# Kernel optimization log

Hardware: AMD Instinct MI355X
Metric: run time of the kernel (lower is better)

## Reference

```python
import jax, jax.numpy as jnp
import numpy as np

B, C, L, O = 32, 256, 336, 96
K, NLAYERS, DFF = 4, 2, 1024
EPS = 1e-5


def setup_inputs() -> dict:
    key = jax.random.key(0)
    ks = jax.random.split(key, 10)
    s1 = 1.0 / np.sqrt(L)
    s2 = 1.0 / np.sqrt(DFF)
    return {
        "x": jax.random.normal(ks[0], (B, C, L), dtype=jnp.float32),
        "rev_w": jnp.ones((C,), dtype=jnp.float32),
        "rev_b": jnp.zeros((C,), dtype=jnp.float32),
        "W1": jax.random.normal(ks[1], (K, NLAYERS, L, DFF), dtype=jnp.float32) * s1,
        "b1": jnp.zeros((K, NLAYERS, DFF), dtype=jnp.float32),
        "W2": jax.random.normal(ks[2], (K, NLAYERS, DFF, L), dtype=jnp.float32) * s2,
        "b2": jnp.zeros((K, NLAYERS, L), dtype=jnp.float32),
        "Wh": jax.random.normal(ks[3], (K, L, O), dtype=jnp.float32) * s1,
        "bh": jnp.zeros((K, O), dtype=jnp.float32),
        "assign": jax.random.randint(ks[4], (C,), 0, K, dtype=jnp.int32),
    }


def reference(x, rev_w, rev_b, W1, b1, W2, b2, Wh, bh, assign):
    # RevIN norm over the time axis, per instance and per channel. x: [B,C,L]
    mean = jnp.mean(x, axis=-1, keepdims=True)
    std = jnp.sqrt(jnp.var(x, axis=-1, keepdims=True) + EPS)
    xn = (x - mean) / std * rev_w[None, :, None] + rev_b[None, :, None]

    n_clusters = Wh.shape[0]
    n_layers = W1.shape[1]
    out = jnp.zeros(x.shape[:2] + (Wh.shape[-1],), dtype=x.dtype)  # [B,C,O]
    for k in range(n_clusters):
        z = xn  # [B,C,L] time-mixing MLP stack shared across channels
        for l in range(n_layers):
            h = jax.nn.relu(jnp.einsum('bcl,ld->bcd', z, W1[k, l]) + b1[k, l])
            z = z + jnp.einsum('bcd,dl->bcl', h, W2[k, l]) + b2[k, l]
        y = jnp.einsum('bcl,lo->bco', z, Wh[k]) + bh[k]  # [B,C,O]
        out = jnp.where((assign == k)[None, :, None], y, out)

    # RevIN denorm, then transpose to [B, out_len, C]
    out = (out - rev_b[None, :, None]) / rev_w[None, :, None] * std + mean
    return jnp.transpose(out, (0, 2, 1))
```

## Files before the change

### kernel.cpp

```cpp
#include <hip/hip_runtime.h>
#include <math.h>


typedef unsigned short u16;
typedef unsigned int u32;
typedef unsigned long long u64;

constexpr int B = 32, C = 256, L = 336, O = 96, K = 4, NL = 2, DFF = 1024;
constexpr int TM = 32;
constexpr int NTILES = (B * C) / TM;
constexpr int LP = 352;
constexpr int KS1 = LP / 32;
constexpr int KS2 = DFF / 32;
constexpr int NT2 = LP / 16;
constexpr int NTH = O / 16;
constexpr int DC = 512;
constexpr int KSC = DC / 32;
constexpr int NTC = DC / 16;
constexpr int ZBS = 360;
constexpr int HSC = DC + 8;

constexpr int W1FRAGS = (DFF / 16) * KS1 * 64;
constexpr int W2FRAGS = NT2 * KS2 * 64;
constexpr int WHFRAGS = NTH * KS1 * 64;
constexpr int NW1 = W1FRAGS * K * NL;
constexpr int NW2 = W2FRAGS * K * NL;
constexpr int NWH = WHFRAGS * K;
constexpr int NFRAG = NW1 + NW2 + NWH;

typedef __bf16 bf16x8 __attribute__((ext_vector_type(8)));
typedef float f32x4 __attribute__((ext_vector_type(4)));

__device__ __forceinline__ u16 f2bf(float f) {
  union { float f; u32 u; } v;
  v.f = f;
  u32 r = v.u + 0x7fffu + ((v.u >> 16) & 1u);
  return (u16)(r >> 16);
}
__device__ __forceinline__ float bf2f(u16 h) {
  union { u32 u; float f; } v;
  v.u = ((u32)h) << 16;
  return v.f;
}

__global__ __launch_bounds__(256) void build_tables(
    const int* __restrict__ assign, int* __restrict__ meta) {
  __shared__ int wcnt[4][K];
  __shared__ int pre[4][K];
  __shared__ int cofs[K + 1];
  const int tid = threadIdx.x;
  const int w = tid >> 6, lane = tid & 63;
  const int a = assign[tid];
  const u64 below = (1ull << lane) - 1ull;
  int myrank = 0;
#pragma unroll
  for (int k = 0; k < K; ++k) {
    const u64 m = __ballot(a == k);
    if (a == k) myrank = (int)__popcll(m & below);
    if (lane == 0) wcnt[w][k] = (int)__popcll(m);
  }
  __syncthreads();
  if (tid == 0) {
    int tot[K];
    for (int k = 0; k < K; ++k) {
      int s = 0;
      for (int ww = 0; ww < 4; ++ww) {
        pre[ww][k] = s;
        s += wcnt[ww][k];
      }
      tot[k] = s;
    }
    cofs[0] = 0;
    for (int k = 0; k < K; ++k) cofs[k + 1] = cofs[k] + tot[k];
    for (int k = 0; k <= K; ++k) meta[512 + k] = cofs[k];
  }
  __syncthreads();
  const int pos = cofs[a] + pre[w][a] + myrank;
  meta[256 + pos] = tid;
  int k = 0;
  while (k < K - 1 && tid >= cofs[k + 1]) ++k;
  meta[tid] = (k << 16) | ((tid - cofs[k]) * TM);
}

__global__ __launch_bounds__(256) void repack(const float* __restrict__ W1,
                                              const float* __restrict__ W2,
                                              const float* __restrict__ Wh,
                                              u16* __restrict__ wbuf) {
  const int gid = blockIdx.x * 256 + threadIdx.x;
  const int lane = gid & 63;
  const int q = lane >> 4, rm = lane & 15;
  float v[8];
  if (gid < NW1) {
    const int kl = gid / W1FRAGS, rem = gid % W1FRAGS;
    const int nt = rem / (KS1 * 64), ks = (rem / 64) % KS1;
    const int d = nt * 16 + rm, lb = ks * 32 + q * 8;
    const float* src = W1 + (size_t)kl * L * DFF;
#pragma unroll
    for (int j = 0; j < 8; ++j) {
      const int l = lb + j;
      v[j] = (l < L) ? src[(size_t)l * DFF + d] : 0.f;
    }
  } else if (gid < NW1 + NW2) {
    const int g = gid - NW1;
    const int kl = g / W2FRAGS, rem = g % W2FRAGS;
    const int nt = rem / (KS2 * 64), ks = (rem / 64) % KS2;
    const int lcol = nt * 16 + rm, db = ks * 32 + q * 8;
    const float* src = W2 + (size_t)kl * DFF * L;
#pragma unroll
    for (int j = 0; j < 8; ++j)
      v[j] = (lcol < L) ? src[(size_t)(db + j) * L + lcol] : 0.f;
  } else {
    const int g = gid - NW1 - NW2;
    const int kk = g / WHFRAGS, rem = g % WHFRAGS;
    const int nt = rem / (KS1 * 64), ks = (rem / 64) % KS1;
    const int o = nt * 16 + rm, lb = ks * 32 + q * 8;
    const float* src = Wh + (size_t)kk * L * O;
#pragma unroll
    for (int j = 0; j < 8; ++j) {
      const int l = lb + j;
      v[j] = (l < L) ? src[(size_t)l * O + o] : 0.f;
    }
  }
  uint4 w;
  w.x = (u32)f2bf(v[0]) | ((u32)f2bf(v[1]) << 16);
  w.y = (u32)f2bf(v[2]) | ((u32)f2bf(v[3]) << 16);
  w.z = (u32)f2bf(v[4]) | ((u32)f2bf(v[5]) << 16);
  w.w = (u32)f2bf(v[6]) | ((u32)f2bf(v[7]) << 16);
  *(uint4*)(wbuf + (size_t)gid * 8) = w;
}

__global__ __launch_bounds__(512, 4) void mlp_mfma(
    const float* __restrict__ x, const float* __restrict__ rev_w,
    const float* __restrict__ rev_b, const float* __restrict__ b1,
    const float* __restrict__ b2, const float* __restrict__ bh,
    const int* __restrict__ meta, const u16* __restrict__ wbuf,
    float* __restrict__ out) {
  __shared__ __align__(16) u16 zb[TM][ZBS];
  __shared__ __align__(16) u16 Hsh[TM][HSC];
  __shared__ float s_mean[TM], s_std[TM], s_rw[TM], s_rb[TM];
  __shared__ int s_b[TM], s_c[TM];

  const int tid = threadIdx.x;
  const int wid = tid >> 6;
  const int lane = tid & 63;
  const int q = lane >> 4, rm = lane & 15;

  const int swz = (blockIdx.x & 7) * 32 + (blockIdx.x >> 3);
  const int info = meta[swz];
  const int kcl = info >> 16;
  const int rstart = info & 0xffff;
  const int cofs = meta[512 + kcl];
  const int cnt = meta[512 + kcl + 1] - cofs;

  for (int i = 0; i < 4; ++i) {
    const int t = wid * 4 + i;
    const int ri = rstart + t;
    const int b = ri / cnt;
    const int c = meta[256 + cofs + (ri % cnt)];
    const float* xrow = x + (size_t)(b * C + c) * L;
    float v[6], s = 0.f, s2 = 0.f;
#pragma unroll
    for (int jj = 0; jj < 6; ++jj) {
      const int j = lane + jj * 64;
      v[jj] = (j < L) ? xrow[j] : 0.f;
      s += v[jj];
      s2 += v[jj] * v[jj];
    }
#pragma unroll
    for (int off = 32; off > 0; off >>= 1) {
      s += __shfl_down(s, off);
      s2 += __shfl_down(s2, off);
    }
    s = __shfl(s, 0);
    s2 = __shfl(s2, 0);
    const float mean = s * (1.f / L);
    const float var = s2 * (1.f / L) - mean * mean;
    const float stdv = sqrtf(var + 1e-5f);
    const float rstd = 1.f / stdv;
    const float rw = rev_w[c], rb_ = rev_b[c];
#pragma unroll
    for (int jj = 0; jj < 6; ++jj) {
      const int j = lane + jj * 64;
      if (j < L) zb[t][j] = f2bf((v[jj] - mean) * rstd * rw + rb_);
    }
    if (lane < LP - L) zb[t][L + lane] = 0;
    if (lane == 0) {
      s_mean[t] = mean;
      s_std[t] = stdv;
      s_rw[t] = rw;
      s_rb[t] = rb_;
      s_b[t] = b;
      s_c[t] = c;
    }
  }
  __syncthreads();

  f32x4 zm[3][2];
#pragma unroll
  for (int t = 0; t < 3; ++t) {
    const int nt2 = wid + 8 * t;
#pragma unroll
    for (int rg = 0; rg < 2; ++rg) {
      if (nt2 < NT2) {
        const uint2 zw = *(const uint2*)&zb[rm + 16 * rg][nt2 * 16 + q * 4];
        zm[t][rg] = f32x4{bf2f((u16)zw.x), bf2f((u16)(zw.x >> 16)),
                          bf2f((u16)zw.y), bf2f((u16)(zw.y >> 16))};
      } else {
        zm[t][rg] = f32x4{0.f, 0.f, 0.f, 0.f};
      }
    }
  }

  const u16* w1b = wbuf;
  const u16* w2b = wbuf + (size_t)NW1 * 8;
  const u16* whb = wbuf + (size_t)(NW1 + NW2) * 8;

  for (int l = 0; l < NL; ++l) {
    const int kl = kcl * NL + l;
    const u16* W1f = w1b + (size_t)kl * W1FRAGS * 8;
    const u16* W2f = w2b + (size_t)kl * W2FRAGS * 8;
    const float* b1p = b1 + kl * DFF;
    const float* b2p = b2 + kl * L;

    for (int cch = 0; cch < 2; ++cch) {
      {
        const u16* base =
            W1f + ((size_t)(cch * NTC + wid * 4) * (KS1 * 512) + lane * 8);
        bf16x8 a_cur[4], a_nxt[4];
#pragma unroll
        for (int t = 0; t < 4; ++t)
          a_cur[t] = *(const bf16x8*)(base + (size_t)t * (KS1 * 512));
        f32x4 acc[4][2];
#pragma unroll
        for (int t = 0; t < 4; ++t)
#pragma unroll
          for (int rg = 0; rg < 2; ++rg) acc[t][rg] = f32x4{0.f, 0.f, 0.f, 0.f};
#pragma unroll 1
        for (int ks = 0; ks < KS1; ++ks) {
          if (ks + 1 < KS1) {
#pragma unroll
            for (int t = 0; t < 4; ++t)
              a_nxt[t] = *(const bf16x8*)(base + (size_t)t * (KS1 * 512) +
                                          (ks + 1) * 512);
          }
          const bf16x8 zf0 = *(const bf16x8*)&zb[rm][ks * 32 + q * 8];
          const bf16x8 zf1 = *(const bf16x8*)&zb[rm + 16][ks * 32 + q * 8];
#pragma unroll
          for (int t = 0; t < 4; ++t) {
            acc[t][0] = __builtin_amdgcn_mfma_f32_16x16x32_bf16(a_cur[t], zf0,
                                                                acc[t][0], 0, 0, 0);
            acc[t][1] = __builtin_amdgcn_mfma_f32_16x16x32_bf16(a_cur[t], zf1,
                                                                acc[t][1], 0, 0, 0);
          }
#pragma unroll
          for (int t = 0; t < 4; ++t) a_cur[t] = a_nxt[t];
        }
#pragma unroll
        for (int t = 0; t < 4; ++t) {
          const int ntl = wid * 4 + t;
          const float4 bq =
              *(const float4*)(b1p + cch * DC + ntl * 16 + q * 4);
#pragma unroll
          for (int rg = 0; rg < 2; ++rg) {
            uint2 hw;
            hw.x = (u32)f2bf(fmaxf(acc[t][rg][0] + bq.x, 0.f)) |
                   ((u32)f2bf(fmaxf(acc[t][rg][1] + bq.y, 0.f)) << 16);
            hw.y = (u32)f2bf(fmaxf(acc[t][rg][2] + bq.z, 0.f)) |
                   ((u32)f2bf(fmaxf(acc[t][rg][3] + bq.w, 0.f)) << 16);
            *(uint2*)&Hsh[rm + 16 * rg][ntl * 16 + q * 4] = hw;
          }
        }
      }
      __syncthreads();

      {
        const u16* b2base = W2f + ((size_t)(cch * KSC) * 512 + lane * 8);
        bf16x8 w_cur[3], w_nxt[3];
#pragma unroll
        for (int t = 0; t < 3; ++t) {
          const int nt2 = wid + 8 * t;
          if (nt2 < NT2)
            w_cur[t] = *(const bf16x8*)(b2base + (size_t)nt2 * (KS2 * 512));
        }
#pragma unroll 1
        for (int ks = 0; ks < KSC; ++ks) {
          if (ks + 1 < KSC) {
#pragma unroll
            for (int t = 0; t < 3; ++t) {
              const int nt2 = wid + 8 * t;
              if (nt2 < NT2)
                w_nxt[t] = *(const bf16x8*)(b2base + (size_t)nt2 * (KS2 * 512) +
                                            (ks + 1) * 512);
            }
          }
          const bf16x8 hf0 = *(const bf16x8*)&Hsh[rm][ks * 32 + q * 8];
          const bf16x8 hf1 = *(const bf16x8*)&Hsh[rm + 16][ks * 32 + q * 8];
#pragma unroll
          for (int t = 0; t < 3; ++t) {
            if (wid + 8 * t < NT2) {
              zm[t][0] = __builtin_amdgcn_mfma_f32_16x16x32_bf16(w_cur[t], hf0,
                                                                 zm[t][0], 0, 0, 0);
              zm[t][1] = __builtin_amdgcn_mfma_f32_16x16x32_bf16(w_cur[t], hf1,
                                                                 zm[t][1], 0, 0, 0);
            }
          }
#pragma unroll
          for (int t = 0; t < 3; ++t) w_cur[t] = w_nxt[t];
        }
      }
      __syncthreads();
    }

#pragma unroll
    for (int t = 0; t < 3; ++t) {
      const int nt2 = wid + 8 * t;
      if (nt2 < NT2) {
        const int lc = nt2 * 16 + q * 4;
        if (lc < L) {
          const float4 bq = *(const float4*)(b2p + lc);
          zm[t][0][0] += bq.x; zm[t][0][1] += bq.y;
          zm[t][0][2] += bq.z; zm[t][0][3] += bq.w;
          zm[t][1][0] += bq.x; zm[t][1][1] += bq.y;
          zm[t][1][2] += bq.z; zm[t][1][3] += bq.w;
        }
#pragma unroll
        for (int rg = 0; rg < 2; ++rg) {
          uint2 zw;
          zw.x = (u32)f2bf(zm[t][rg][0]) | ((u32)f2bf(zm[t][rg][1]) << 16);
          zw.y = (u32)f2bf(zm[t][rg][2]) | ((u32)f2bf(zm[t][rg][3]) << 16);
          *(uint2*)&zb[rm + 16 * rg][lc] = zw;
        }
      }
    }
    __syncthreads();
  }

  if (wid < NTH) {
    const u16* Whf =
        whb + (size_t)kcl * WHFRAGS * 8 + (size_t)wid * (KS1 * 512) + lane * 8;
    f32x4 acc0 = {0.f, 0.f, 0.f, 0.f}, acc1 = {0.f, 0.f, 0.f, 0.f};
    for (int ks = 0; ks < KS1; ++ks) {
      const bf16x8 af = *(const bf16x8*)(Whf + ks * 512);
      const bf16x8 zf0 = *(const bf16x8*)&zb[rm][ks * 32 + q * 8];
      const bf16x8 zf1 = *(const bf16x8*)&zb[rm + 16][ks * 32 + q * 8];
      acc0 = __builtin_amdgcn_mfma_f32_16x16x32_bf16(af, zf0, acc0, 0, 0, 0);
      acc1 = __builtin_amdgcn_mfma_f32_16x16x32_bf16(af, zf1, acc1, 0, 0, 0);
    }
    const float4 bq = *(const float4*)(bh + kcl * O + wid * 16 + q * 4);
    const float bqa[4] = {bq.x, bq.y, bq.z, bq.w};
#pragma unroll
    for (int rg = 0; rg < 2; ++rg) {
      const int row = rm + 16 * rg;
      const float mean = s_mean[row], stdv = s_std[row];
      const float rw = s_rw[row], rb_ = s_rb[row];
      const int ob = s_b[row], oc = s_c[row];
      const f32x4 acc = rg ? acc1 : acc0;
#pragma unroll
      for (int gg = 0; gg < 4; ++gg) {
        const int o = wid * 16 + q * 4 + gg;
        const float y = acc[gg] + bqa[gg];
        out[((size_t)ob * O + o) * C + oc] = (y - rb_) / rw * stdv + mean;
      }
    }
  }
}

extern "C" void kernel_launch(void* const* d_in, const int* in_sizes, int n_in,
                              void* d_out, int out_size, void* d_ws,
                              size_t ws_size, hipStream_t stream) {
  const float* x = (const float*)d_in[0];
  const float* rev_w = (const float*)d_in[1];
  const float* rev_b = (const float*)d_in[2];
  const float* W1 = (const float*)d_in[3];
  const float* b1 = (const float*)d_in[4];
  const float* W2 = (const float*)d_in[5];
  const float* b2 = (const float*)d_in[6];
  const float* Wh = (const float*)d_in[7];
  const float* bh = (const float*)d_in[8];
  const int* assign = (const int*)d_in[9];
  float* out = (float*)d_out;

  int* meta = (int*)d_ws;
  u16* wbuf = (u16*)((char*)d_ws + 4096);

  build_tables<<<1, 256, 0, stream>>>(assign, meta);
  repack<<<NFRAG / 256, 256, 0, stream>>>(W1, W2, Wh, wbuf);
  mlp_mfma<<<NTILES, 512, 0, stream>>>(x, rev_w, rev_b, b1, b2, bh, meta, wbuf,
                                       out);
}
```

Measured before the change: 165.8 us.

## Coalesce weight repack via LDS transpose and deepen MFMA weight prefetch

Splits the weight repack into three kernels that read rows with coalesced float4 loads, transpose through shared memory, and write MFMA fragment layout, replacing strided scalar gathers. The main kernel drops the two-chunk DFF split and computes the full 1024-wide hidden layer into a larger shared H buffer with 8 tiles per wave. Weight prefetch becomes two stages deep for W1 and three for W2, and the next layer's W1 loads are issued before the layer-end barrier. This removes a barrier per chunk and hides global latency, at the cost of more registers and LDS, so launch bounds drop to 2 blocks per SM, which lowers occupancy.

```diff
diff --git a/kernel.cpp b/kernel.cpp
--- a/kernel.cpp
+++ b/kernel.cpp
@@ -14,19 +14,14 @@
 constexpr int KS2 = DFF / 32;
 constexpr int NT2 = LP / 16;
 constexpr int NTH = O / 16;
-constexpr int DC = 512;
-constexpr int KSC = DC / 32;
-constexpr int NTC = DC / 16;
 constexpr int ZBS = 360;
-constexpr int HSC = DC + 8;
+constexpr int HS = 1032;
 
 constexpr int W1FRAGS = (DFF / 16) * KS1 * 64;
 constexpr int W2FRAGS = NT2 * KS2 * 64;
 constexpr int WHFRAGS = NTH * KS1 * 64;
 constexpr int NW1 = W1FRAGS * K * NL;
 constexpr int NW2 = W2FRAGS * K * NL;
-constexpr int NWH = WHFRAGS * K;
-constexpr int NFRAG = NW1 + NW2 + NWH;
 
 typedef __bf16 bf16x8 __attribute__((ext_vector_type(8)));
 typedef float f32x4 __attribute__((ext_vector_type(4)));
@@ -41,6 +36,9 @@
   union { u32 u; float f; } v;
   v.u = ((u32)h) << 16;
   return v.f;
+}
+__device__ __forceinline__ u32 pack2(float a, float b) {
+  return (u32)f2bf(a) | ((u32)f2bf(b) << 16);
 }
 
 __global__ __launch_bounds__(256) void build_tables(
@@ -82,61 +80,140 @@
   meta[tid] = (k << 16) | ((tid - cofs[k]) * TM);
 }
 
-__global__ __launch_bounds__(256) void repack(const float* __restrict__ W1,
-                                              const float* __restrict__ W2,
-                                              const float* __restrict__ Wh,
-                                              u16* __restrict__ wbuf) {
-  const int gid = blockIdx.x * 256 + threadIdx.x;
-  const int lane = gid & 63;
+
+__global__ __launch_bounds__(256) void repack_w1(const float* __restrict__ W1,
+                                                 u16* __restrict__ wbuf) {
+  __shared__ u16 sm[32][516];
+  const int tid = threadIdx.x;
+  const int wid = tid >> 6, lane = tid & 63;
+  const int dh = blockIdx.x & 1;
+  const int ks = (blockIdx.x >> 1) % 11;
+  const int kl = blockIdx.x / 22;
+  for (int rr = 0; rr < 8; ++rr) {
+    const int r = wid * 8 + rr;
+    const int l = ks * 32 + r;
+#pragma unroll
+    for (int h = 0; h < 2; ++h) {
+      const int c = h * 256 + lane * 4;
+      float4 v = make_float4(0.f, 0.f, 0.f, 0.f);
+      if (l < L)
+        v = *(const float4*)(W1 + ((size_t)kl * L + l) * DFF + dh * 512 + c);
+      uint2 p;
+      p.x = pack2(v.x, v.y);
+      p.y = pack2(v.z, v.w);
+      *(uint2*)&sm[r][c] = p;
+    }
+  }
+  __syncthreads();
   const int q = lane >> 4, rm = lane & 15;
-  float v[8];
-  if (gid < NW1) {
-    const int kl = gid / W1FRAGS, rem = gid % W1FRAGS;
-    const int nt = rem / (KS1 * 64), ks = (rem / 64) % KS1;
-    const int d = nt * 16 + rm, lb = ks * 32 + q * 8;
-    const float* src = W1 + (size_t)kl * L * DFF;
-#pragma unroll
-    for (int j = 0; j < 8; ++j) {
-      const int l = lb + j;
-      v[j] = (l < L) ? src[(size_t)l * DFF + d] : 0.f;
-    }
-  } else if (gid < NW1 + NW2) {
-    const int g = gid - NW1;
-    const int kl = g / W2FRAGS, rem = g % W2FRAGS;
-    const int nt = rem / (KS2 * 64), ks = (rem / 64) % KS2;
-    const int lcol = nt * 16 + rm, db = ks * 32 + q * 8;
-    const float* src = W2 + (size_t)kl * DFF * L;
-#pragma unroll
-    for (int j = 0; j < 8; ++j)
-      v[j] = (lcol < L) ? src[(size_t)(db + j) * L + lcol] : 0.f;
-  } else {
-    const int g = gid - NW1 - NW2;
-    const int kk = g / WHFRAGS, rem = g % WHFRAGS;
-    const int nt = rem / (KS1 * 64), ks = (rem / 64) % KS1;
-    const int o = nt * 16 + rm, lb = ks * 32 + q * 8;
-    const float* src = Wh + (size_t)kk * L * O;
-#pragma unroll
-    for (int j = 0; j < 8; ++j) {
-      const int l = lb + j;
-      v[j] = (l < L) ? src[(size_t)l * O + o] : 0.f;
-    }
-  }
-  uint4 w;
-  w.x = (u32)f2bf(v[0]) | ((u32)f2bf(v[1]) << 16);
-  w.y = (u32)f2bf(v[2]) | ((u32)f2bf(v[3]) << 16);
-  w.z = (u32)f2bf(v[4]) | ((u32)f2bf(v[5]) << 16);
-  w.w = (u32)f2bf(v[6]) | ((u32)f2bf(v[7]) << 16);
-  *(uint4*)(wbuf + (size_t)gid * 8) = w;
-}
-
-__global__ __launch_bounds__(512, 4) void mlp_mfma(
+  for (int e = 0; e < 8; ++e) {
+    const int ntl = wid * 8 + e;
+    const int nt = dh * 32 + ntl;
+    uint4 o;
+    u32 w4[4];
+#pragma unroll
+    for (int jj = 0; jj < 4; ++jj) {
+      const u16 a = sm[q * 8 + 2 * jj][ntl * 16 + rm];
+      const u16 b = sm[q * 8 + 2 * jj + 1][ntl * 16 + rm];
+      w4[jj] = (u32)a | ((u32)b << 16);
+    }
+    o.x = w4[0]; o.y = w4[1]; o.z = w4[2]; o.w = w4[3];
+    *(uint4*)(wbuf + ((size_t)(kl * 64 + nt) * 11 + ks) * 512 + lane * 8) = o;
+  }
+}
+
+__global__ __launch_bounds__(256) void repack_w2(const float* __restrict__ W2,
+                                                 u16* __restrict__ wbuf) {
+  __shared__ u16 sm[32][356];
+  const int tid = threadIdx.x;
+  const int wid = tid >> 6, lane = tid & 63;
+  const int ks = blockIdx.x & 31;
+  const int kl = blockIdx.x >> 5;
+  for (int rr = 0; rr < 8; ++rr) {
+    const int r = wid * 8 + rr;
+    const float* row = W2 + ((size_t)kl * DFF + ks * 32 + r) * L;
+    {
+      const int c = lane * 4;
+      const float4 v = *(const float4*)(row + c);
+      uint2 p;
+      p.x = pack2(v.x, v.y);
+      p.y = pack2(v.z, v.w);
+      *(uint2*)&sm[r][c] = p;
+    }
+    {
+      const int c = 256 + lane * 4;
+      if (c < 352) {
+        float4 v = make_float4(0.f, 0.f, 0.f, 0.f);
+        if (c < L) v = *(const float4*)(row + c);
+        uint2 p;
+        p.x = pack2(v.x, v.y);
+        p.y = pack2(v.z, v.w);
+        *(uint2*)&sm[r][c] = p;
+      }
+    }
+  }
+  __syncthreads();
+  const int q = lane >> 4, rm = lane & 15;
+  for (int nt = wid; nt < NT2; nt += 4) {
+    u32 w4[4];
+#pragma unroll
+    for (int jj = 0; jj < 4; ++jj) {
+      const u16 a = sm[q * 8 + 2 * jj][nt * 16 + rm];
+      const u16 b = sm[q * 8 + 2 * jj + 1][nt * 16 + rm];
+      w4[jj] = (u32)a | ((u32)b << 16);
+    }
+    uint4 o;
+    o.x = w4[0]; o.y = w4[1]; o.z = w4[2]; o.w = w4[3];
+    *(uint4*)(wbuf + (size_t)NW1 * 8 +
+              ((size_t)(kl * 22 + nt) * 32 + ks) * 512 + lane * 8) = o;
+  }
+}
+
+__global__ __launch_bounds__(256) void repack_wh(const float* __restrict__ Wh,
+                                                 u16* __restrict__ wbuf) {
+  __shared__ u16 sm[32][100];
+  const int tid = threadIdx.x;
+  const int wid = tid >> 6, lane = tid & 63;
+  const int ks = blockIdx.x % 11;
+  const int kk = blockIdx.x / 11;
+  for (int rr = 0; rr < 8; ++rr) {
+    const int r = wid * 8 + rr;
+    const int l = ks * 32 + r;
+    if (lane < 24) {
+      const int c = lane * 4;
+      float4 v = make_float4(0.f, 0.f, 0.f, 0.f);
+      if (l < L) v = *(const float4*)(Wh + ((size_t)kk * L + l) * O + c);
+      uint2 p;
+      p.x = pack2(v.x, v.y);
+      p.y = pack2(v.z, v.w);
+      *(uint2*)&sm[r][c] = p;
+    }
+  }
+  __syncthreads();
+  const int q = lane >> 4, rm = lane & 15;
+  for (int nt = wid; nt < NTH; nt += 4) {
+    u32 w4[4];
+#pragma unroll
+    for (int jj = 0; jj < 4; ++jj) {
+      const u16 a = sm[q * 8 + 2 * jj][nt * 16 + rm];
+      const u16 b = sm[q * 8 + 2 * jj + 1][nt * 16 + rm];
+      w4[jj] = (u32)a | ((u32)b << 16);
+    }
+    uint4 o;
+    o.x = w4[0]; o.y = w4[1]; o.z = w4[2]; o.w = w4[3];
+    *(uint4*)(wbuf + (size_t)(NW1 + NW2) * 8 +
+              ((size_t)(kk * 6 + nt) * 11 + ks) * 512 + lane * 8) = o;
+  }
+}
+
+__global__ __launch_bounds__(512, 2) void mlp_mfma(
     const float* __restrict__ x, const float* __restrict__ rev_w,
     const float* __restrict__ rev_b, const float* __restrict__ b1,
     const float* __restrict__ b2, const float* __restrict__ bh,
     const int* __restrict__ meta, const u16* __restrict__ wbuf,
     float* __restrict__ out) {
   __shared__ __align__(16) u16 zb[TM][ZBS];
-  __shared__ __align__(16) u16 Hsh[TM][HSC];
+  __shared__ __align__(16) u16 Hsh[TM][HS];
   __shared__ float s_mean[TM], s_std[TM], s_rw[TM], s_rb[TM];
   __shared__ int s_b[TM], s_c[TM];
 
@@ -193,6 +270,23 @@
       s_c[t] = c;
     }
   }
+
+  const u16* w1b = wbuf;
+  const u16* w2b = wbuf + (size_t)NW1 * 8;
+  const u16* whb = wbuf + (size_t)(NW1 + NW2) * 8;
+  constexpr int TS1 = KS1 * 512;
+  constexpr int TS2 = KS2 * 512;
+
+  bf16x8 acur[8], anxt[8];
+  {
+    const u16* base =
+        w1b + (size_t)(kcl * NL) * W1FRAGS * 8 + (size_t)(wid * 8) * TS1 + lane * 8;
+#pragma unroll
+    for (int t = 0; t < 8; ++t) {
+      acur[t] = *(const bf16x8*)(base + (size_t)t * TS1);
+      anxt[t] = *(const bf16x8*)(base + (size_t)t * TS1 + 512);
+    }
+  }
   __syncthreads();
 
   f32x4 zm[3][2];
@@ -211,104 +305,98 @@
     }
   }
 
-  const u16* w1b = wbuf;
-  const u16* w2b = wbuf + (size_t)NW1 * 8;
-  const u16* whb = wbuf + (size_t)(NW1 + NW2) * 8;
-
   for (int l = 0; l < NL; ++l) {
     const int kl = kcl * NL + l;
     const u16* W1f = w1b + (size_t)kl * W1FRAGS * 8;
     const u16* W2f = w2b + (size_t)kl * W2FRAGS * 8;
     const float* b1p = b1 + kl * DFF;
     const float* b2p = b2 + kl * L;
-
-    for (int cch = 0; cch < 2; ++cch) {
-      {
-        const u16* base =
-            W1f + ((size_t)(cch * NTC + wid * 4) * (KS1 * 512) + lane * 8);
-        bf16x8 a_cur[4], a_nxt[4];
-#pragma unroll
-        for (int t = 0; t < 4; ++t)
-          a_cur[t] = *(const bf16x8*)(base + (size_t)t * (KS1 * 512));
-        f32x4 acc[4][2];
-#pragma unroll
-        for (int t = 0; t < 4; ++t)
-#pragma unroll
-          for (int rg = 0; rg < 2; ++rg) acc[t][rg] = f32x4{0.f, 0.f, 0.f, 0.f};
-#pragma unroll 1
-        for (int ks = 0; ks < KS1; ++ks) {
-          if (ks + 1 < KS1) {
-#pragma unroll
-            for (int t = 0; t < 4; ++t)
-              a_nxt[t] = *(const bf16x8*)(base + (size_t)t * (KS1 * 512) +
-                                          (ks + 1) * 512);
-          }
-          const bf16x8 zf0 = *(const bf16x8*)&zb[rm][ks * 32 + q * 8];
-          const bf16x8 zf1 = *(const bf16x8*)&zb[rm + 16][ks * 32 + q * 8];
-#pragma unroll
-          for (int t = 0; t < 4; ++t) {
-            acc[t][0] = __builtin_amdgcn_mfma_f32_16x16x32_bf16(a_cur[t], zf0,
-                                                                acc[t][0], 0, 0, 0);
-            acc[t][1] = __builtin_amdgcn_mfma_f32_16x16x32_bf16(a_cur[t], zf1,
-                                                                acc[t][1], 0, 0, 0);
-          }
-#pragma unroll
-          for (int t = 0; t < 4; ++t) a_cur[t] = a_nxt[t];
-        }
-#pragma unroll
-        for (int t = 0; t < 4; ++t) {
-          const int ntl = wid * 4 + t;
-          const float4 bq =
-              *(const float4*)(b1p + cch * DC + ntl * 16 + q * 4);
-#pragma unroll
-          for (int rg = 0; rg < 2; ++rg) {
-            uint2 hw;
-            hw.x = (u32)f2bf(fmaxf(acc[t][rg][0] + bq.x, 0.f)) |
-                   ((u32)f2bf(fmaxf(acc[t][rg][1] + bq.y, 0.f)) << 16);
-            hw.y = (u32)f2bf(fmaxf(acc[t][rg][2] + bq.z, 0.f)) |
-                   ((u32)f2bf(fmaxf(acc[t][rg][3] + bq.w, 0.f)) << 16);
-            *(uint2*)&Hsh[rm + 16 * rg][ntl * 16 + q * 4] = hw;
-          }
-        }
-      }
-      __syncthreads();
-
-      {
-        const u16* b2base = W2f + ((size_t)(cch * KSC) * 512 + lane * 8);
-        bf16x8 w_cur[3], w_nxt[3];
+    const u16* base1 = W1f + (size_t)(wid * 8) * TS1 + lane * 8;
+
+    f32x4 acc[8][2];
+#pragma unroll
+    for (int t = 0; t < 8; ++t)
+#pragma unroll
+      for (int rg = 0; rg < 2; ++rg) acc[t][rg] = f32x4{0.f, 0.f, 0.f, 0.f};
+#pragma unroll 2
+    for (int ks = 0; ks < KS1; ++ks) {
+      bf16x8 ause[8];
+#pragma unroll
+      for (int t = 0; t < 8; ++t) {
+        ause[t] = acur[t];
+        acur[t] = anxt[t];
+      }
+      if (ks + 2 < KS1) {
+#pragma unroll
+        for (int t = 0; t < 8; ++t)
+          anxt[t] = *(const bf16x8*)(base1 + (size_t)t * TS1 + (ks + 2) * 512);
+      }
+      const bf16x8 zf0 = *(const bf16x8*)&zb[rm][ks * 32 + q * 8];
+      const bf16x8 zf1 = *(const bf16x8*)&zb[rm + 16][ks * 32 + q * 8];
+#pragma unroll
+      for (int t = 0; t < 8; ++t) {
+        acc[t][0] =
+            __builtin_amdgcn_mfma_f32_16x16x32_bf16(ause[t], zf0, acc[t][0], 0, 0, 0);
+        acc[t][1] =
+            __builtin_amdgcn_mfma_f32_16x16x32_bf16(ause[t], zf1, acc[t][1], 0, 0, 0);
+      }
+    }
+#pragma unroll
+    for (int t = 0; t < 8; ++t) {
+      const int nt = wid * 8 + t;
+      const float4 bq = *(const float4*)(b1p + nt * 16 + q * 4);
+#pragma unroll
+      for (int rg = 0; rg < 2; ++rg) {
+        uint2 hw;
+        hw.x = pack2(fmaxf(acc[t][rg][0] + bq.x, 0.f),
+                     fmaxf(acc[t][rg][1] + bq.y, 0.f));
+        hw.y = pack2(fmaxf(acc[t][rg][2] + bq.z, 0.f),
+                     fmaxf(acc[t][rg][3] + bq.w, 0.f));
+        *(uint2*)&Hsh[rm + 16 * rg][nt * 16 + q * 4] = hw;
+      }
+    }
+
+    const u16* base2 = W2f + lane * 8;
+    bf16x8 wq0[3], wq1[3], wq2[3];
+#pragma unroll
+    for (int t = 0; t < 3; ++t) {
+      const int nt2 = wid + 8 * t;
+      if (nt2 < NT2) {
+        wq0[t] = *(const bf16x8*)(base2 + (size_t)nt2 * TS2);
+        wq1[t] = *(const bf16x8*)(base2 + (size_t)nt2 * TS2 + 512);
+        wq2[t] = *(const bf16x8*)(base2 + (size_t)nt2 * TS2 + 1024);
+      }
+    }
+    __syncthreads();
+
+#pragma unroll 2
+    for (int ks = 0; ks < KS2; ++ks) {
+      bf16x8 wuse[3];
+#pragma unroll
+      for (int t = 0; t < 3; ++t) {
+        wuse[t] = wq0[t];
+        wq0[t] = wq1[t];
+        wq1[t] = wq2[t];
+      }
+      if (ks + 3 < KS2) {
 #pragma unroll
         for (int t = 0; t < 3; ++t) {
           const int nt2 = wid + 8 * t;
           if (nt2 < NT2)
-            w_cur[t] = *(const bf16x8*)(b2base + (size_t)nt2 * (KS2 * 512));
+            wq2[t] = *(const bf16x8*)(base2 + (size_t)nt2 * TS2 + (ks + 3) * 512);
         }
-#pragma unroll 1
-        for (int ks = 0; ks < KSC; ++ks) {
-          if (ks + 1 < KSC) {
-#pragma unroll
-            for (int t = 0; t < 3; ++t) {
-              const int nt2 = wid + 8 * t;
-              if (nt2 < NT2)
-                w_nxt[t] = *(const bf16x8*)(b2base + (size_t)nt2 * (KS2 * 512) +
-                                            (ks + 1) * 512);
-            }
-          }
-          const bf16x8 hf0 = *(const bf16x8*)&Hsh[rm][ks * 32 + q * 8];
-          const bf16x8 hf1 = *(const bf16x8*)&Hsh[rm + 16][ks * 32 + q * 8];
-#pragma unroll
-          for (int t = 0; t < 3; ++t) {
-            if (wid + 8 * t < NT2) {
-              zm[t][0] = __builtin_amdgcn_mfma_f32_16x16x32_bf16(w_cur[t], hf0,
-                                                                 zm[t][0], 0, 0, 0);
-              zm[t][1] = __builtin_amdgcn_mfma_f32_16x16x32_bf16(w_cur[t], hf1,
-                                                                 zm[t][1], 0, 0, 0);
-            }
-          }
-#pragma unroll
-          for (int t = 0; t < 3; ++t) w_cur[t] = w_nxt[t];
+      }
+      const bf16x8 hf0 = *(const bf16x8*)&Hsh[rm][ks * 32 + q * 8];
+      const bf16x8 hf1 = *(const bf16x8*)&Hsh[rm + 16][ks * 32 + q * 8];
+#pragma unroll
+      for (int t = 0; t < 3; ++t) {
+        if (wid + 8 * t < NT2) {
+          zm[t][0] =
+              __builtin_amdgcn_mfma_f32_16x16x32_bf16(wuse[t], hf0, zm[t][0], 0, 0, 0);
+          zm[t][1] =
+              __builtin_amdgcn_mfma_f32_16x16x32_bf16(wuse[t], hf1, zm[t][1], 0, 0, 0);
         }
       }
-      __syncthreads();
     }
 
 #pragma unroll
@@ -326,18 +414,28 @@
 #pragma unroll
         for (int rg = 0; rg < 2; ++rg) {
           uint2 zw;
-          zw.x = (u32)f2bf(zm[t][rg][0]) | ((u32)f2bf(zm[t][rg][1]) << 16);
-          zw.y = (u32)f2bf(zm[t][rg][2]) | ((u32)f2bf(zm[t][rg][3]) << 16);
+          zw.x = pack2(zm[t][rg][0], zm[t][rg][1]);
+          zw.y = pack2(zm[t][rg][2], zm[t][rg][3]);
           *(uint2*)&zb[rm + 16 * rg][lc] = zw;
         }
       }
     }
+
+    if (l + 1 < NL) {
+      const u16* nb = w1b + (size_t)(kl + 1) * W1FRAGS * 8 +
+                      (size_t)(wid * 8) * TS1 + lane * 8;
+#pragma unroll
+      for (int t = 0; t < 8; ++t) {
+        acur[t] = *(const bf16x8*)(nb + (size_t)t * TS1);
+        anxt[t] = *(const bf16x8*)(nb + (size_t)t * TS1 + 512);
+      }
+    }
     __syncthreads();
   }
 
   if (wid < NTH) {
     const u16* Whf =
-        whb + (size_t)kcl * WHFRAGS * 8 + (size_t)wid * (KS1 * 512) + lane * 8;
+        whb + (size_t)kcl * WHFRAGS * 8 + (size_t)wid * TS1 + lane * 8;
     f32x4 acc0 = {0.f, 0.f, 0.f, 0.f}, acc1 = {0.f, 0.f, 0.f, 0.f};
     for (int ks = 0; ks < KS1; ++ks) {
       const bf16x8 af = *(const bf16x8*)(Whf + ks * 512);
@@ -384,7 +482,9 @@
   u16* wbuf = (u16*)((char*)d_ws + 4096);
 
   build_tables<<<1, 256, 0, stream>>>(assign, meta);
-  repack<<<NFRAG / 256, 256, 0, stream>>>(W1, W2, Wh, wbuf);
+  repack_w1<<<K * NL * 11 * 2, 256, 0, stream>>>(W1, wbuf);
+  repack_w2<<<K * NL * 32, 256, 0, stream>>>(W2, wbuf);
+  repack_wh<<<K * 11, 256, 0, stream>>>(Wh, wbuf);
   mlp_mfma<<<NTILES, 512, 0, stream>>>(x, rev_w, rev_b, b1, b2, bh, meta, wbuf,
                                        out);
 }
```

Measured after the change: 177.8 us. 1.07x slower.
